# Optimization experiments

Measured on AMD Instinct MI355X. Metric: run time of the kernel, lower is better.

## Reference

```python
import jax, jax.numpy as jnp
import numpy as np

D_MODEL = 1024
N_HEADS = 16
D_HEAD = D_MODEL // N_HEADS
B, T = 2, 2048


def setup_inputs() -> dict:
    key = jax.random.key(0)
    k1, k2, k3 = jax.random.split(key, 3)
    x = jax.random.normal(k1, (B, T, D_MODEL), dtype=jnp.float32)
    # torch nn.Linear weights: y = x @ W.T, W has shape [out, in]
    W_qkv = jax.random.normal(k2, (3 * D_MODEL, D_MODEL), dtype=jnp.float32) * (1.0 / np.sqrt(D_MODEL))
    W_out = jax.random.normal(k3, (D_MODEL, D_MODEL), dtype=jnp.float32) * (1.0 / np.sqrt(D_MODEL))
    return {"x": x, "W_qkv": W_qkv, "W_out": W_out}


def reference(x, W_qkv, W_out):
    Bb, Tt, Dd = x.shape
    qkv = (x @ W_qkv.T).reshape(Bb, Tt, 3, N_HEADS, D_HEAD)
    q, k, v = qkv[:, :, 0], qkv[:, :, 1], qkv[:, :, 2]  # [B,T,H,d]
    q = q.transpose(0, 2, 1, 3)  # [B,H,T,d]
    k = k.transpose(0, 2, 1, 3)
    v = v.transpose(0, 2, 1, 3)
    scale = 1.0 / np.sqrt(D_HEAD)
    scores = jnp.einsum('bhqd,bhkd->bhqk', q, k) * scale  # [B,H,T,T]
    causal = jnp.tril(jnp.ones((Tt, Tt), dtype=bool))
    scores = jnp.where(causal, scores, -jnp.inf)
    A = jax.nn.softmax(scores, axis=-1)
    AV = jnp.einsum('bhqk,bhkd->bhqd', A, v)
    AAV = jnp.einsum('bhqk,bhkd->bhqd', A, AV)  # twicing correction
    out = 2.0 * AV - AAV  # [B,H,T,d]
    out = out.transpose(0, 2, 1, 3).reshape(Bb, Tt, Dd)
    return out @ W_out.T
```

## Files before the change

kernel.cpp:

```cpp
#include <hip/hip_runtime.h>
#include <hip/hip_bf16.h>

#define T_SEQ  2048
#define DMODEL 1024
#define NH     16
#define DH     64
#define NTOK   4096
#define QSCALE 0.18033688011112042f
#define M_FIX  16.0f

typedef unsigned short u16;
typedef short s16x8 __attribute__((ext_vector_type(8)));
typedef unsigned short u16x8 __attribute__((ext_vector_type(8)));
typedef float f32x4 __attribute__((ext_vector_type(4)));

__device__ __forceinline__ u16 f2bf(float f) {
  unsigned u = __float_as_uint(f);
  u += 0x7FFFu + ((u >> 16) & 1u);
  return (u16)(u >> 16);
}
__device__ __forceinline__ unsigned pk2(float a, float b) {
  __hip_bfloat162 h = __float22bfloat162_rn(make_float2(a, b));
  unsigned u;
  __builtin_memcpy(&u, &h, 4);
  return u;
}
__device__ __forceinline__ unsigned pk2z(float a, float b) {
  return __builtin_amdgcn_perm(__float_as_uint(b), __float_as_uint(a), 0x07060302);
}
__device__ __forceinline__ float bf2f(u16 x) {
  return __uint_as_float(((unsigned)x) << 16);
}
__device__ __forceinline__ void async_cp16(const u16* g, u16* l) {
  __builtin_amdgcn_global_load_lds(
      (const __attribute__((address_space(1))) unsigned*)g,
      (__attribute__((address_space(3))) unsigned*)l, 16, 0, 0);
}

__global__ void cast_all(const float* __restrict__ x, const float* __restrict__ wqkv,
                         const float* __restrict__ wout, u16* __restrict__ out) {
  int i = blockIdx.x * blockDim.x + threadIdx.x;
  const float* src; int off;
  if (i < 1048576)      { src = x;    off = 0; }
  else if (i < 1835008) { src = wqkv; off = 1048576; }
  else                  { src = wout; off = 1835008; }
  float4 v = reinterpret_cast<const float4*>(src)[i - off];
  ushort4 r;
  r.x = f2bf(v.x); r.y = f2bf(v.y); r.z = f2bf(v.z); r.w = f2bf(v.w);
  reinterpret_cast<ushort4*>(out)[i] = r;
}

__global__ __launch_bounds__(512, 2) void gemm_qkv(
    const u16* __restrict__ A, const u16* __restrict__ Bm,
    u16* __restrict__ outQ, u16* __restrict__ outK, u16* __restrict__ outV) {
  __shared__ __align__(16) u16 SM[65536];
  const int tid = threadIdx.x, wave = tid >> 6, lane = tid & 63;
  const int f15 = lane & 15, quad = lane >> 4;
  const int bm = blockIdx.x * 256, bn = blockIdx.y * 256;
  const int wm = wave >> 2, wn = wave & 3;
  const int K = DMODEL;

  f32x4 acc[8][4] = {};

  const u16* Ag0 = A  + (size_t)(bm + (2 * wave) * 16 + f15) * K + quad * 8;
  const u16* Ag1 = A  + (size_t)(bm + (2 * wave + 1) * 16 + f15) * K + quad * 8;
  const u16* Bg0 = Bm + (size_t)(bn + (2 * wave) * 16 + f15) * K + quad * 8;
  const u16* Bg1 = Bm + (size_t)(bn + (2 * wave + 1) * 16 + f15) * K + quad * 8;
  u16* LA0 = SM + (2 * wave) * 512 + lane * 8;
  u16* LA1 = SM + (2 * wave + 1) * 512 + lane * 8;
  u16* LB0 = SM + 8192 + (2 * wave) * 512 + lane * 8;
  u16* LB1 = SM + 8192 + (2 * wave + 1) * 512 + lane * 8;

  const int S = K >> 5;
#pragma unroll
  for (int s = 0; s < 3; s++) {
    const int k0 = s * 32, o = s * 16384;
    async_cp16(Ag0 + k0, LA0 + o); async_cp16(Ag1 + k0, LA1 + o);
    async_cp16(Bg0 + k0, LB0 + o); async_cp16(Bg1 + k0, LB1 + o);
  }

  for (int s = 0; s < S; s++) {
    if (s < S - 2)       asm volatile("s_waitcnt vmcnt(8)" ::: "memory");
    else if (s == S - 2) asm volatile("s_waitcnt vmcnt(4)" ::: "memory");
    else                 asm volatile("s_waitcnt vmcnt(0)" ::: "memory");
    __builtin_amdgcn_s_barrier();
    __builtin_amdgcn_sched_barrier(0);
    if (s + 3 < S) {
      const int k0 = (s + 3) * 32, o = ((s + 3) & 3) * 16384;
      async_cp16(Ag0 + k0, LA0 + o); async_cp16(Ag1 + k0, LA1 + o);
      async_cp16(Bg0 + k0, LB0 + o); async_cp16(Bg1 + k0, LB1 + o);
    }
    const u16* Sl = SM + (s & 3) * 16384;
    s16x8 af[8], bfr[4];
#pragma unroll
    for (int ni = 0; ni < 4; ni++)
      bfr[ni] = *reinterpret_cast<const s16x8*>(Sl + 8192 + (wn * 4 + ni) * 512 + lane * 8);
#pragma unroll
    for (int mi = 0; mi < 8; mi++)
      af[mi] = *reinterpret_cast<const s16x8*>(Sl + (wm * 8 + mi) * 512 + lane * 8);
    __builtin_amdgcn_s_setprio(1);
#pragma unroll
    for (int mi = 0; mi < 8; mi++)
#pragma unroll
      for (int ni = 0; ni < 4; ni++)
        acc[mi][ni] = __builtin_amdgcn_mfma_f32_16x16x32_bf16(af[mi], bfr[ni], acc[mi][ni], 0, 0, 0);
    __builtin_amdgcn_s_setprio(0);
  }

  __syncthreads();
  u16* Cs = SM;
  const int ST = 264;
  if (bn < 2048) {
    const float scale = (bn < 1024) ? QSCALE : 1.0f;
#pragma unroll
    for (int c = 0; c < 4; c++) {
      if (c) __syncthreads();
      if (wm == (c >> 1)) {
#pragma unroll
        for (int mi2 = 0; mi2 < 4; mi2++) {
          const int mi = (c & 1) * 4 + mi2;
#pragma unroll
          for (int ni = 0; ni < 4; ni++) {
            const int col = (wn * 4 + ni) * 16 + f15;
#pragma unroll
            for (int r = 0; r < 4; r++)
              Cs[(mi2 * 16 + quad * 4 + r) * ST + col] = f2bf(acc[mi][ni][r] * scale);
          }
        }
      }
      __syncthreads();
      const int row = tid >> 3, cb = (tid & 7) * 32;
      const int gm = bm + c * 64 + row;
#pragma unroll
      for (int c8 = 0; c8 < 4; c8++) {
        const int gc = bn + cb + c8 * 8;
        u16x8 v = *reinterpret_cast<const u16x8*>(&Cs[row * ST + cb + c8 * 8]);
        const int which = gc >> 10, hh = (gc >> 6) & 15, d = gc & 63;
        u16* dst = (which ? outK : outQ) + ((size_t)hh * NTOK + gm) * 64 + d;
        *reinterpret_cast<u16x8*>(dst) = v;
      }
    }
  } else {
    const int bnV = bn - 2048;
#pragma unroll
    for (int c = 0; c < 4; c++) {
      if (c) __syncthreads();
      if (wm == (c >> 1)) {
#pragma unroll
        for (int mi2 = 0; mi2 < 4; mi2++) {
          const int mi = (c & 1) * 4 + mi2;
#pragma unroll
          for (int ni = 0; ni < 4; ni++) {
            const int col = (wn * 4 + ni) * 16 + f15;
#pragma unroll
            for (int r = 0; r < 4; r++)
              Cs[(mi2 * 16 + quad * 4 + r) * ST + col] = f2bf(acc[mi][ni][r]);
          }
        }
      }
      __syncthreads();
      const int fc = tid >> 3, s8 = (tid & 7) * 8;
      const int tb = ((s8 >> 5) & 1) * 32 + ((s8 >> 3) & 3) * 4;
      const int gmb = bm + c * 64;
#pragma unroll
      for (int p = 0; p < 4; p++) {
        const int d = p * 64 + fc;
        u16x8 vv;
#pragma unroll
        for (int j = 0; j < 4; j++) vv[j] = Cs[(tb + j) * ST + d];
#pragma unroll
        for (int j = 0; j < 4; j++) vv[4 + j] = Cs[(tb + 16 + j) * ST + d];
        *reinterpret_cast<u16x8*>(outV + (size_t)(bnV + d) * NTOK + gmb + s8) = vv;
      }
    }
  }
}

__global__ __launch_bounds__(256) void gemm_out(
    const u16* __restrict__ A, const u16* __restrict__ Bm, float* __restrict__ outF) {
  __shared__ __align__(16) u16 SM[18432];
  const int tid = threadIdx.x, wave = tid >> 6, lane = tid & 63;
  const int f15 = lane & 15, quad = lane >> 4;
  const int bm = blockIdx.x * 64, bn = blockIdx.y * 128;
  const int wr = wave >> 1, wc = wave & 1;
  const int K = DMODEL, N = DMODEL;

  f32x4 acc[2][4] = {};

  const u16* Ag = A  + (size_t)(bm + wave * 16 + f15) * K + quad * 8;
  const u16* Bg0 = Bm + (size_t)(bn + (2 * wave) * 16 + f15) * K + quad * 8;
  const u16* Bg1 = Bm + (size_t)(bn + (2 * wave + 1) * 16 + f15) * K + quad * 8;
  u16* LA  = SM + wave * 512 + lane * 8;
  u16* LB0 = SM + 2048 + (2 * wave) * 512 + lane * 8;
  u16* LB1 = SM + 2048 + (2 * wave + 1) * 512 + lane * 8;

  const int KT = K >> 5;
  async_cp16(Ag, LA); async_cp16(Bg0, LB0); async_cp16(Bg1, LB1);
  async_cp16(Ag + 32, LA + 6144); async_cp16(Bg0 + 32, LB0 + 6144); async_cp16(Bg1 + 32, LB1 + 6144);

  int bufr = 0, bufw = 2;
  for (int kt = 0; kt < KT; kt++) {
    if (kt + 1 < KT) asm volatile("s_waitcnt vmcnt(3)" ::: "memory");
    else             asm volatile("s_waitcnt vmcnt(0)" ::: "memory");
    __builtin_amdgcn_s_barrier();
    __builtin_amdgcn_sched_barrier(0);
    if (kt + 2 < KT) {
      const int k0 = (kt + 2) * 32;
      const int o = bufw * 6144;
      async_cp16(Ag + k0, LA + o); async_cp16(Bg0 + k0, LB0 + o); async_cp16(Bg1 + k0, LB1 + o);
    }
    const u16* Af = SM + bufr * 6144;
    const u16* Bf = Af + 2048;
    s16x8 af[2], bfr[4];
#pragma unroll
    for (int mi = 0; mi < 2; mi++)
      af[mi] = *reinterpret_cast<const s16x8*>(Af + (wr * 2 + mi) * 512 + lane * 8);
#pragma unroll
    for (int ni = 0; ni < 4; ni++)
      bfr[ni] = *reinterpret_cast<const s16x8*>(Bf + (wc * 4 + ni) * 512 + lane * 8);
#pragma unroll
    for (int mi = 0; mi < 2; mi++)
#pragma unroll
      for (int ni = 0; ni < 4; ni++)
        acc[mi][ni] = __builtin_amdgcn_mfma_f32_16x16x32_bf16(af[mi], bfr[ni], acc[mi][ni], 0, 0, 0);
    bufr = (bufr == 2) ? 0 : bufr + 1;
    bufw = (bufw == 2) ? 0 : bufw + 1;
  }

#pragma unroll
  for (int mi = 0; mi < 2; mi++)
#pragma unroll
    for (int ni = 0; ni < 4; ni++)
#pragma unroll
      for (int r = 0; r < 4; r++)
        outF[(size_t)(bm + wr * 32 + mi * 16 + quad * 4 + r) * N + bn + wc * 64 + ni * 16 + f15] =
            acc[mi][ni][r];
}

template <int PASS>
__global__ __launch_bounds__(256) void attn_pass(
    const u16* __restrict__ Qb, const u16* __restrict__ Kb, const u16* __restrict__ Vsrc,
    float* __restrict__ LinvG, u16* __restrict__ Vp2, u16* __restrict__ TW) {
  __shared__ __align__(16) u16 SM[16384];
  const int tid = threadIdx.x, wave = tid >> 6, lane = tid & 63;
  const int f15 = lane & 15, quad = lane >> 4;
  const int bid = blockIdx.x;
  const int y = (bid & 7) * 4 + ((bid >> 3) & 3);
  const int b = y >> 4, h = y & 15;
  const int g = bid >> 5;
  const int qt2 = (g < 8) ? (15 - g) : (g - 8);
  const int q0 = qt2 * 128;
  const int ntiles = 2 * qt2 + 2;
  const size_t qk_base = ((size_t)h * NTOK + (size_t)b * T_SEQ) * 64;
  const size_t vt_base = (size_t)h * 64 * NTOK + (size_t)b * T_SEQ;

  s16x8 qf[2][2];
#pragma unroll
  for (int grp = 0; grp < 2; grp++) {
    const u16* qp = Qb + qk_base + (size_t)(q0 + 32 * wave + 16 * grp + f15) * 64 + quad * 8;
    qf[grp][0] = *reinterpret_cast<const s16x8*>(qp);
    qf[grp][1] = *reinterpret_cast<const s16x8*>(qp + 32);
  }
  float invl[2] = {0.f, 0.f};
  if (PASS == 1) {
#pragma unroll
    for (int grp = 0; grp < 2; grp++)
      invl[grp] = LinvG[(size_t)y * T_SEQ + q0 + 32 * wave + 16 * grp + f15];
  }

  f32x4 accO[2][4] = {};
  float l_acc[2] = {0.f, 0.f};

  const u16* Kg = Kb  + qk_base + (size_t)(wave * 16 + f15) * 64 + quad * 8;
  const u16* Vg = Vsrc + vt_base + (size_t)(wave * 16 + f15) * NTOK + quad * 8;
  u16* LK = SM + (wave * 2) * 512 + lane * 8;
  u16* LV = SM + 4096 + (wave * 2) * 512 + lane * 8;

  async_cp16(Kg, LK); async_cp16(Kg + 32, LK + 512);
  async_cp16(Vg, LV); async_cp16(Vg + 32, LV + 512);
  __syncthreads();

  for (int ti = 0; ti < ntiles; ti++) {
    const int buf = ti & 1;
    if (ti + 1 < ntiles) {
      const int j1 = (ti + 1) * 64;
      const int o = (buf ^ 1) * 8192;
      async_cp16(Kg + (size_t)j1 * 64, LK + o);
      async_cp16(Kg + (size_t)j1 * 64 + 32, LK + o + 512);
      async_cp16(Vg + j1, LV + o);
      async_cp16(Vg + j1 + 32, LV + o + 512);
    }
    const u16* Kf = SM + buf * 8192;
    const u16* Vf = SM + buf * 8192 + 4096;
    const int D = (ti - 2 * qt2) * 64;

    if (D < 32 * wave + 32) {
      f32x4 accS[2][4] = {};
#pragma unroll
      for (int st = 0; st < 4; st++) {
        s16x8 k0 = *reinterpret_cast<const s16x8*>(Kf + (st * 2) * 512 + lane * 8);
        s16x8 k1 = *reinterpret_cast<const s16x8*>(Kf + (st * 2 + 1) * 512 + lane * 8);
#pragma unroll
        for (int grp = 0; grp < 2; grp++) {
          accS[grp][st] = __builtin_amdgcn_mfma_f32_16x16x32_bf16(k0, qf[grp][0], accS[grp][st], 0, 0, 0);
          accS[grp][st] = __builtin_amdgcn_mfma_f32_16x16x32_bf16(k1, qf[grp][1], accS[grp][st], 0, 0, 0);
        }
      }
      union pbu { s16x8 v; unsigned u[4]; } pb[2][2];
      if (D + 63 <= 32 * wave) {
#pragma unroll
        for (int grp = 0; grp < 2; grp++)
#pragma unroll
          for (int st = 0; st < 4; st++) {
            float e0 = __builtin_amdgcn_exp2f(accS[grp][st][0] - M_FIX);
            float e1 = __builtin_amdgcn_exp2f(accS[grp][st][1] - M_FIX);
            float e2 = __builtin_amdgcn_exp2f(accS[grp][st][2] - M_FIX);
            float e3 = __builtin_amdgcn_exp2f(accS[grp][st][3] - M_FIX);
            if (PASS == 0) l_acc[grp] += (e0 + e1) + (e2 + e3);
            unsigned w0 = pk2z(e0, e1), w1 = pk2z(e2, e3);
            if (st < 2) { pb[grp][0].u[(st & 1) * 2] = w0; pb[grp][0].u[(st & 1) * 2 + 1] = w1; }
            else        { pb[grp][1].u[(st & 1) * 2] = w0; pb[grp][1].u[(st & 1) * 2 + 1] = w1; }
          }
      } else {
#pragma unroll
        for (int grp = 0; grp < 2; grp++) {
          const int qrel = 32 * wave + 16 * grp + f15;
#pragma unroll
          for (int st = 0; st < 4; st++) {
            const int jb = D + st * 16 + quad * 4;
            float e0 = (jb + 0 <= qrel) ? __builtin_amdgcn_exp2f(accS[grp][st][0] - M_FIX) : 0.f;
            float e1 = (jb + 1 <= qrel) ? __builtin_amdgcn_exp2f(accS[grp][st][1] - M_FIX) : 0.f;
            float e2 = (jb + 2 <= qrel) ? __builtin_amdgcn_exp2f(accS[grp][st][2] - M_FIX) : 0.f;
            float e3 = (jb + 3 <= qrel) ? __builtin_amdgcn_exp2f(accS[grp][st][3] - M_FIX) : 0.f;
            if (PASS == 0) l_acc[grp] += (e0 + e1) + (e2 + e3);
            unsigned w0 = pk2z(e0, e1), w1 = pk2z(e2, e3);
            if (st < 2) { pb[grp][0].u[(st & 1) * 2] = w0; pb[grp][0].u[(st & 1) * 2 + 1] = w1; }
            else        { pb[grp][1].u[(st & 1) * 2] = w0; pb[grp][1].u[(st & 1) * 2 + 1] = w1; }
          }
        }
      }
#pragma unroll
      for (int mt = 0; mt < 4; mt++) {
        s16x8 v0 = *reinterpret_cast<const s16x8*>(Vf + (mt * 2) * 512 + lane * 8);
        s16x8 v1 = *reinterpret_cast<const s16x8*>(Vf + (mt * 2 + 1) * 512 + lane * 8);
#pragma unroll
        for (int grp = 0; grp < 2; grp++) {
          accO[grp][mt] = __builtin_amdgcn_mfma_f32_16x16x32_bf16(v0, pb[grp][0].v, accO[grp][mt], 0, 0, 0);
          accO[grp][mt] = __builtin_amdgcn_mfma_f32_16x16x32_bf16(v1, pb[grp][1].v, accO[grp][mt], 0, 0, 0);
        }
      }
    }
    __syncthreads();
  }

  if (PASS == 0) {
#pragma unroll
    for (int grp = 0; grp < 2; grp++) {
      float l = l_acc[grp];
      l += __shfl_xor(l, 16);
      l += __shfl_xor(l, 32);
      invl[grp] = 1.0f / l;
      if (quad == 0) LinvG[(size_t)y * T_SEQ + q0 + 32 * wave + 16 * grp + f15] = invl[grp];
    }
  }

  if (PASS == 0) {
    u16* E = SM;
#pragma unroll
    for (int g64 = 0; g64 < 2; g64++) {
      __syncthreads();
      if ((wave >> 1) == g64) {
#pragma unroll
        for (int grp = 0; grp < 2; grp++) {
          const int ql = 32 * (wave & 1) + 16 * grp + f15;
          const int slot = (ql >> 5) * 32 + ((ql >> 2) & 3) * 8 + ((ql >> 4) & 1) * 4 + (ql & 3);
#pragma unroll
          for (int mt = 0; mt < 4; mt++)
#pragma unroll
            for (int r = 0; r < 4; r++)
              E[(mt * 16 + quad * 4 + r) * 68 + slot] = f2bf(accO[grp][mt][r] * invl[grp]);
        }
      }
      __syncthreads();
      const int d = tid >> 2, s = (tid & 3) * 16;
      const u16* vg2 = Vsrc + vt_base + (size_t)d * NTOK + q0 + 64 * g64 + s;
      u16* og = Vp2 + vt_base + (size_t)d * NTOK + q0 + 64 * g64 + s;
#pragma unroll
      for (int g2 = 0; g2 < 2; g2++) {
        u16x8 vv = *reinterpret_cast<const u16x8*>(vg2 + g2 * 8);
        u16x8 ee = *reinterpret_cast<const u16x8*>(&E[d * 68 + s + g2 * 8]);
        u16x8 oo;
#pragma unroll
        for (int i = 0; i < 8; i++) oo[i] = f2bf(2.0f * bf2f(vv[i]) - bf2f(ee[i]));
        *reinterpret_cast<u16x8*>(og + g2 * 8) = oo;
      }
    }
  } else {
    u16* E2 = SM;
#pragma unroll
    for (int g64 = 0; g64 < 2; g64++) {
      __syncthreads();
      if ((wave >> 1) == g64) {
#pragma unroll
        for (int grp = 0; grp < 2; grp++) {
          const int ql = 32 * (wave & 1) + 16 * grp + f15;
#pragma unroll
          for (int mt = 0; mt < 4; mt++) {
            uint2 w;
            w.x = pk2(accO[grp][mt][0] * invl[grp], accO[grp][mt][1] * invl[grp]);
            w.y = pk2(accO[grp][mt][2] * invl[grp], accO[grp][mt][3] * invl[grp]);
            *reinterpret_cast<uint2*>(&E2[ql * 72 + mt * 16 + quad * 4]) = w;
          }
        }
      }
      __syncthreads();
      const int q = tid >> 2, s = (tid & 3) * 16;
      u16* dst = TW + ((size_t)b * T_SEQ + q0 + 64 * g64 + q) * DMODEL + h * 64 + s;
      *reinterpret_cast<u16x8*>(dst) = *reinterpret_cast<const u16x8*>(&E2[q * 72 + s]);
      *reinterpret_cast<u16x8*>(dst + 8) = *reinterpret_cast<const u16x8*>(&E2[q * 72 + s + 8]);
    }
  }
}

extern "C" void kernel_launch(void* const* d_in, const int* in_sizes, int n_in,
                              void* d_out, int out_size, void* d_ws, size_t ws_size,
                              hipStream_t stream) {
  const float* x    = (const float*)d_in[0];
  const float* Wqkv = (const float*)d_in[1];
  const float* Wout = (const float*)d_in[2];
  float* out = (float*)d_out;
  char* ws = (char*)d_ws;

  u16*   Xb    = (u16*)(ws + 0);
  u16*   Wqkvb = (u16*)(ws + 8388608);
  u16*   Woutb = (u16*)(ws + 14680064);
  u16*   Qb    = (u16*)(ws + 16777216);
  u16*   Kb    = (u16*)(ws + 25165824);
  u16*   Vtp   = (u16*)(ws + 33554432);
  u16*   TW    = (u16*)(ws + 41943040);
  u16*   Vp2   = (u16*)(ws + 50331648);
  float* LinvG = (float*)(ws + 58720256);

  cast_all<<<8192, 256, 0, stream>>>(x, Wqkv, Wout, Xb);

  gemm_qkv<<<dim3(16, 12), 512, 0, stream>>>(Xb, Wqkvb, Qb, Kb, Vtp);

  attn_pass<0><<<512, 256, 0, stream>>>(Qb, Kb, Vtp, LinvG, Vp2, nullptr);
  attn_pass<1><<<512, 256, 0, stream>>>(Qb, Kb, Vp2, LinvG, nullptr, TW);

  gemm_out<<<dim3(64, 8), 256, 0, stream>>>(TW, Woutb, out);
}
```

Measured before the change: 220.6 us.

## Triple-buffer K/V tiles in attention pass with one barrier per iteration

Changes the attention K/V staging from double to triple buffering, prefetching two tiles ahead with partial vmcnt waits. It keeps a single barrier per iteration instead of a __syncthreads after compute, which lets loads overlap compute more deeply. The cost is 48KB of LDS instead of 32KB, which may reduce occupancy, and correctness now depends on the vmcnt counting being exact.

```diff
diff --git a/kernel.cpp b/kernel.cpp
--- a/kernel.cpp
+++ b/kernel.cpp
@@ -241,7 +241,7 @@
 __global__ __launch_bounds__(256) void attn_pass(
     const u16* __restrict__ Qb, const u16* __restrict__ Kb, const u16* __restrict__ Vsrc,
     float* __restrict__ LinvG, u16* __restrict__ Vp2, u16* __restrict__ TW) {
-  __shared__ __align__(16) u16 SM[16384];
+  __shared__ __align__(16) u16 SM[24576];
   const int tid = threadIdx.x, wave = tid >> 6, lane = tid & 63;
   const int f15 = lane & 15, quad = lane >> 4;
   const int bid = blockIdx.x;
@@ -276,22 +276,26 @@
   u16* LK = SM + (wave * 2) * 512 + lane * 8;
   u16* LV = SM + 4096 + (wave * 2) * 512 + lane * 8;
 
-  async_cp16(Kg, LK); async_cp16(Kg + 32, LK + 512);
-  async_cp16(Vg, LV); async_cp16(Vg + 32, LV + 512);
-  __syncthreads();
+#define ATTN_STAGE(t_) do { \
+    const int j_ = (t_) * 64, o_ = ((t_) % 3) * 8192; \
+    async_cp16(Kg + (size_t)j_ * 64, LK + o_); \
+    async_cp16(Kg + (size_t)j_ * 64 + 32, LK + o_ + 512); \
+    async_cp16(Vg + j_, LV + o_); \
+    async_cp16(Vg + j_ + 32, LV + o_ + 512); \
+  } while (0)
+
+  ATTN_STAGE(0);
+  ATTN_STAGE(1);
 
   for (int ti = 0; ti < ntiles; ti++) {
-    const int buf = ti & 1;
-    if (ti + 1 < ntiles) {
-      const int j1 = (ti + 1) * 64;
-      const int o = (buf ^ 1) * 8192;
-      async_cp16(Kg + (size_t)j1 * 64, LK + o);
-      async_cp16(Kg + (size_t)j1 * 64 + 32, LK + o + 512);
-      async_cp16(Vg + j1, LV + o);
-      async_cp16(Vg + j1 + 32, LV + o + 512);
-    }
-    const u16* Kf = SM + buf * 8192;
-    const u16* Vf = SM + buf * 8192 + 4096;
+    if (ti + 1 < ntiles) asm volatile("s_waitcnt vmcnt(4)" ::: "memory");
+    else                 asm volatile("s_waitcnt vmcnt(0)" ::: "memory");
+    __builtin_amdgcn_s_barrier();
+    __builtin_amdgcn_sched_barrier(0);
+    if (ti + 2 < ntiles) ATTN_STAGE(ti + 2);
+
+    const u16* Kf = SM + (ti % 3) * 8192;
+    const u16* Vf = Kf + 4096;
     const int D = (ti - 2 * qt2) * 64;
 
     if (D < 32 * wave + 32) {
@@ -350,8 +354,8 @@
         }
       }
     }
-    __syncthreads();
-  }
+  }
+#undef ATTN_STAGE
 
   if (PASS == 0) {
 #pragma unroll
```

New measurement: 223.6 us. About the same (+1.4%).

## Restructure QKV GEMM main loop into ping-pong double-stage schedule with interleaved barriers

Applied to the files above, without the earlier changes.

Reworks the QKV projection GEMM k-loop to process two k-stages per iteration. A-fragment LDS reads are split into four sub-phases, each followed by a barrier, so waves alternate between LDS reads and MFMA bursts. Async global-to-LDS copies for the next two stages are issued together once per outer iteration. The aim is to overlap LDS traffic and MFMA across waves and cut per-stage waitcnt overhead, at the cost of many more barriers and a more fragile wait-count schedule.

```diff
diff --git a/kernel.cpp b/kernel.cpp
--- a/kernel.cpp
+++ b/kernel.cpp
@@ -71,41 +71,63 @@
   u16* LB0 = SM + 8192 + (2 * wave) * 512 + lane * 8;
   u16* LB1 = SM + 8192 + (2 * wave + 1) * 512 + lane * 8;
 
-  const int S = K >> 5;
-#pragma unroll
-  for (int s = 0; s < 3; s++) {
-    const int k0 = s * 32, o = s * 16384;
-    async_cp16(Ag0 + k0, LA0 + o); async_cp16(Ag1 + k0, LA1 + o);
-    async_cp16(Bg0 + k0, LB0 + o); async_cp16(Bg1 + k0, LB1 + o);
-  }
-
-  for (int s = 0; s < S; s++) {
-    if (s < S - 2)       asm volatile("s_waitcnt vmcnt(8)" ::: "memory");
-    else if (s == S - 2) asm volatile("s_waitcnt vmcnt(4)" ::: "memory");
-    else                 asm volatile("s_waitcnt vmcnt(0)" ::: "memory");
-    __builtin_amdgcn_s_barrier();
-    __builtin_amdgcn_sched_barrier(0);
-    if (s + 3 < S) {
-      const int k0 = (s + 3) * 32, o = ((s + 3) & 3) * 16384;
-      async_cp16(Ag0 + k0, LA0 + o); async_cp16(Ag1 + k0, LA1 + o);
-      async_cp16(Bg0 + k0, LB0 + o); async_cp16(Bg1 + k0, LB1 + o);
-    }
-    const u16* Sl = SM + (s & 3) * 16384;
-    s16x8 af[8], bfr[4];
-#pragma unroll
-    for (int ni = 0; ni < 4; ni++)
-      bfr[ni] = *reinterpret_cast<const s16x8*>(Sl + 8192 + (wn * 4 + ni) * 512 + lane * 8);
-#pragma unroll
-    for (int mi = 0; mi < 8; mi++)
-      af[mi] = *reinterpret_cast<const s16x8*>(Sl + (wm * 8 + mi) * 512 + lane * 8);
-    __builtin_amdgcn_s_setprio(1);
-#pragma unroll
-    for (int mi = 0; mi < 8; mi++)
-#pragma unroll
-      for (int ni = 0; ni < 4; ni++)
-        acc[mi][ni] = __builtin_amdgcn_mfma_f32_16x16x32_bf16(af[mi], bfr[ni], acc[mi][ni], 0, 0, 0);
-    __builtin_amdgcn_s_setprio(0);
-  }
+#define QKV_STAGE(s_) do { \
+    const int k0_ = (s_) * 32, o_ = ((s_) & 3) * 16384; \
+    async_cp16(Ag0 + k0_, LA0 + o_); async_cp16(Ag1 + k0_, LA1 + o_); \
+    async_cp16(Bg0 + k0_, LB0 + o_); async_cp16(Bg1 + k0_, LB1 + o_); \
+  } while (0)
+
+  QKV_STAGE(0); QKV_STAGE(1); QKV_STAGE(2); QKV_STAGE(3);
+  asm volatile("s_waitcnt vmcnt(8)" ::: "memory");
+  __builtin_amdgcn_s_barrier();
+  __builtin_amdgcn_sched_barrier(0);
+
+  for (int T = 0; T < 16; T++) {
+    const u16* S0 = SM + ((2 * T) & 3) * 16384;
+    const u16* S1 = SM + ((2 * T + 1) & 3) * 16384;
+    s16x8 bfr0[4], bfr1[4];
+#pragma unroll
+    for (int ni = 0; ni < 4; ni++) {
+      bfr0[ni] = *reinterpret_cast<const s16x8*>(S0 + 8192 + (wn * 4 + ni) * 512 + lane * 8);
+      bfr1[ni] = *reinterpret_cast<const s16x8*>(S1 + 8192 + (wn * 4 + ni) * 512 + lane * 8);
+    }
+#pragma unroll
+    for (int q = 0; q < 4; q++) {
+      s16x8 a00 = *reinterpret_cast<const s16x8*>(S0 + (wm * 8 + 2 * q) * 512 + lane * 8);
+      s16x8 a10 = *reinterpret_cast<const s16x8*>(S0 + (wm * 8 + 2 * q + 1) * 512 + lane * 8);
+      s16x8 a01 = *reinterpret_cast<const s16x8*>(S1 + (wm * 8 + 2 * q) * 512 + lane * 8);
+      s16x8 a11 = *reinterpret_cast<const s16x8*>(S1 + (wm * 8 + 2 * q + 1) * 512 + lane * 8);
+      asm volatile("s_waitcnt lgkmcnt(0)" ::: "memory");
+      __builtin_amdgcn_s_barrier();
+      if (q == 3) {
+        __builtin_amdgcn_sched_barrier(0);
+        if (T <= 13) { QKV_STAGE(2 * T + 4); QKV_STAGE(2 * T + 5); }
+      }
+      __builtin_amdgcn_s_setprio(1);
+#pragma unroll
+      for (int ni = 0; ni < 4; ni++) {
+        acc[2 * q][ni]     = __builtin_amdgcn_mfma_f32_16x16x32_bf16(a00, bfr0[ni], acc[2 * q][ni], 0, 0, 0);
+        acc[2 * q + 1][ni] = __builtin_amdgcn_mfma_f32_16x16x32_bf16(a10, bfr0[ni], acc[2 * q + 1][ni], 0, 0, 0);
+      }
+#pragma unroll
+      for (int ni = 0; ni < 4; ni++) {
+        acc[2 * q][ni]     = __builtin_amdgcn_mfma_f32_16x16x32_bf16(a01, bfr1[ni], acc[2 * q][ni], 0, 0, 0);
+        acc[2 * q + 1][ni] = __builtin_amdgcn_mfma_f32_16x16x32_bf16(a11, bfr1[ni], acc[2 * q + 1][ni], 0, 0, 0);
+      }
+      __builtin_amdgcn_s_setprio(0);
+      if (q < 3) {
+        __builtin_amdgcn_s_barrier();
+      } else {
+        if (T <= 13)      asm volatile("s_waitcnt vmcnt(8)" ::: "memory");
+        else if (T == 14) asm volatile("s_waitcnt vmcnt(0)" ::: "memory");
+        if (T < 15) {
+          __builtin_amdgcn_s_barrier();
+          __builtin_amdgcn_sched_barrier(0);
+        }
+      }
+    }
+  }
+#undef QKV_STAGE
 
   __syncthreads();
   u16* Cs = SM;
```

Result: slower. 231.5 us (+4.9%).

## Shrink QKV GEMM N-tile to 192 to fill more CUs

Applied to the files above, without the earlier changes.

The QKV projection GEMM's N-tile shrinks from 256 to 192 columns, raising the grid from 192 to 256 blocks so all CUs on the MI355X get work instead of leaving many idle. The load schedule, wait counts and LDS layout are reworked because waves now load unequal amounts of B. The epilogue is merged so a tile can straddle the K/V boundary, with Q scaling applied per column. In exchange each block does less reuse per K-step and the epilogue has more branching.

```diff
diff --git a/kernel.cpp b/kernel.cpp
--- a/kernel.cpp
+++ b/kernel.cpp
@@ -53,48 +53,54 @@
 __global__ __launch_bounds__(512, 2) void gemm_qkv(
     const u16* __restrict__ A, const u16* __restrict__ Bm,
     u16* __restrict__ outQ, u16* __restrict__ outK, u16* __restrict__ outV) {
-  __shared__ __align__(16) u16 SM[65536];
+  __shared__ __align__(16) u16 SM[57344];
   const int tid = threadIdx.x, wave = tid >> 6, lane = tid & 63;
   const int f15 = lane & 15, quad = lane >> 4;
-  const int bm = blockIdx.x * 256, bn = blockIdx.y * 256;
+  const int bm = blockIdx.x * 256, bn = blockIdx.y * 192;
   const int wm = wave >> 2, wn = wave & 3;
   const int K = DMODEL;
 
-  f32x4 acc[8][4] = {};
-
-  const u16* Ag0 = A  + (size_t)(bm + (2 * wave) * 16 + f15) * K + quad * 8;
-  const u16* Ag1 = A  + (size_t)(bm + (2 * wave + 1) * 16 + f15) * K + quad * 8;
-  const u16* Bg0 = Bm + (size_t)(bn + (2 * wave) * 16 + f15) * K + quad * 8;
-  const u16* Bg1 = Bm + (size_t)(bn + (2 * wave + 1) * 16 + f15) * K + quad * 8;
+  f32x4 acc[8][3] = {};
+
+  const u16* Ag0 = A + (size_t)(bm + (2 * wave) * 16 + f15) * K + quad * 8;
+  const u16* Ag1 = A + (size_t)(bm + (2 * wave + 1) * 16 + f15) * K + quad * 8;
+  const int bf0 = (wave < 4) ? (2 * wave) : (wave + 4);
+  const int bf1 = 2 * wave + 1;
+  const u16* Bg0 = Bm + (size_t)(bn + bf0 * 16 + f15) * K + quad * 8;
+  const u16* Bg1 = Bm + (size_t)(bn + bf1 * 16 + f15) * K + quad * 8;
   u16* LA0 = SM + (2 * wave) * 512 + lane * 8;
   u16* LA1 = SM + (2 * wave + 1) * 512 + lane * 8;
-  u16* LB0 = SM + 8192 + (2 * wave) * 512 + lane * 8;
-  u16* LB1 = SM + 8192 + (2 * wave + 1) * 512 + lane * 8;
+  u16* LB0 = SM + 8192 + bf0 * 512 + lane * 8;
+  u16* LB1 = SM + 8192 + bf1 * 512 + lane * 8;
+
+#define QKV_STAGE(s_) do { \
+    const int k0_ = (s_) * 32, o_ = ((s_) & 3) * 14336; \
+    async_cp16(Ag0 + k0_, LA0 + o_); async_cp16(Ag1 + k0_, LA1 + o_); \
+    async_cp16(Bg0 + k0_, LB0 + o_); \
+    if (wave < 4) async_cp16(Bg1 + k0_, LB1 + o_); \
+  } while (0)
 
   const int S = K >> 5;
-#pragma unroll
-  for (int s = 0; s < 3; s++) {
-    const int k0 = s * 32, o = s * 16384;
-    async_cp16(Ag0 + k0, LA0 + o); async_cp16(Ag1 + k0, LA1 + o);
-    async_cp16(Bg0 + k0, LB0 + o); async_cp16(Bg1 + k0, LB1 + o);
-  }
+  QKV_STAGE(0); QKV_STAGE(1); QKV_STAGE(2);
 
   for (int s = 0; s < S; s++) {
-    if (s < S - 2)       asm volatile("s_waitcnt vmcnt(8)" ::: "memory");
-    else if (s == S - 2) asm volatile("s_waitcnt vmcnt(4)" ::: "memory");
-    else                 asm volatile("s_waitcnt vmcnt(0)" ::: "memory");
+    if (s < S - 2) {
+      if (wave < 4) asm volatile("s_waitcnt vmcnt(8)" ::: "memory");
+      else          asm volatile("s_waitcnt vmcnt(6)" ::: "memory");
+    } else if (s == S - 2) {
+      if (wave < 4) asm volatile("s_waitcnt vmcnt(4)" ::: "memory");
+      else          asm volatile("s_waitcnt vmcnt(3)" ::: "memory");
+    } else {
+      asm volatile("s_waitcnt vmcnt(0)" ::: "memory");
+    }
     __builtin_amdgcn_s_barrier();
     __builtin_amdgcn_sched_barrier(0);
-    if (s + 3 < S) {
-      const int k0 = (s + 3) * 32, o = ((s + 3) & 3) * 16384;
-      async_cp16(Ag0 + k0, LA0 + o); async_cp16(Ag1 + k0, LA1 + o);
-      async_cp16(Bg0 + k0, LB0 + o); async_cp16(Bg1 + k0, LB1 + o);
-    }
-    const u16* Sl = SM + (s & 3) * 16384;
-    s16x8 af[8], bfr[4];
-#pragma unroll
-    for (int ni = 0; ni < 4; ni++)
-      bfr[ni] = *reinterpret_cast<const s16x8*>(Sl + 8192 + (wn * 4 + ni) * 512 + lane * 8);
+    if (s + 3 < S) QKV_STAGE(s + 3);
+    const u16* Sl = SM + (s & 3) * 14336;
+    s16x8 af[8], bfr[3];
+#pragma unroll
+    for (int ni = 0; ni < 3; ni++)
+      bfr[ni] = *reinterpret_cast<const s16x8*>(Sl + 8192 + (wn * 3 + ni) * 512 + lane * 8);
 #pragma unroll
     for (int mi = 0; mi < 8; mi++)
       af[mi] = *reinterpret_cast<const s16x8*>(Sl + (wm * 8 + mi) * 512 + lane * 8);
@@ -102,75 +108,65 @@
 #pragma unroll
     for (int mi = 0; mi < 8; mi++)
 #pragma unroll
-      for (int ni = 0; ni < 4; ni++)
+      for (int ni = 0; ni < 3; ni++)
         acc[mi][ni] = __builtin_amdgcn_mfma_f32_16x16x32_bf16(af[mi], bfr[ni], acc[mi][ni], 0, 0, 0);
     __builtin_amdgcn_s_setprio(0);
   }
+#undef QKV_STAGE
 
   __syncthreads();
   u16* Cs = SM;
-  const int ST = 264;
-  if (bn < 2048) {
-    const float scale = (bn < 1024) ? QSCALE : 1.0f;
-#pragma unroll
-    for (int c = 0; c < 4; c++) {
-      if (c) __syncthreads();
-      if (wm == (c >> 1)) {
-#pragma unroll
-        for (int mi2 = 0; mi2 < 4; mi2++) {
-          const int mi = (c & 1) * 4 + mi2;
-#pragma unroll
-          for (int ni = 0; ni < 4; ni++) {
-            const int col = (wn * 4 + ni) * 16 + f15;
-#pragma unroll
-            for (int r = 0; r < 4; r++)
-              Cs[(mi2 * 16 + quad * 4 + r) * ST + col] = f2bf(acc[mi][ni][r] * scale);
-          }
-        }
-      }
-      __syncthreads();
-      const int row = tid >> 3, cb = (tid & 7) * 32;
+  const int ST = 200;
+  const bool hasQK = (bn < 2048);
+  const bool hasV  = (bn + 192 > 2048);
+#pragma unroll
+  for (int c = 0; c < 4; c++) {
+    if (c) __syncthreads();
+    if (wm == (c >> 1)) {
+#pragma unroll
+      for (int mi2 = 0; mi2 < 4; mi2++) {
+        const int mi = (c & 1) * 4 + mi2;
+#pragma unroll
+        for (int ni = 0; ni < 3; ni++) {
+          const int col = (wn * 3 + ni) * 16 + f15;
+          const float sc = (bn + col < 1024) ? QSCALE : 1.0f;
+#pragma unroll
+          for (int r = 0; r < 4; r++)
+            Cs[(mi2 * 16 + quad * 4 + r) * ST + col] = f2bf(acc[mi][ni][r] * sc);
+        }
+      }
+    }
+    __syncthreads();
+    if (hasQK) {
+      const int row = tid >> 3, cs = (tid & 7) * 24;
       const int gm = bm + c * 64 + row;
 #pragma unroll
-      for (int c8 = 0; c8 < 4; c8++) {
-        const int gc = bn + cb + c8 * 8;
-        u16x8 v = *reinterpret_cast<const u16x8*>(&Cs[row * ST + cb + c8 * 8]);
-        const int which = gc >> 10, hh = (gc >> 6) & 15, d = gc & 63;
-        u16* dst = (which ? outK : outQ) + ((size_t)hh * NTOK + gm) * 64 + d;
-        *reinterpret_cast<u16x8*>(dst) = v;
-      }
-    }
-  } else {
-    const int bnV = bn - 2048;
-#pragma unroll
-    for (int c = 0; c < 4; c++) {
-      if (c) __syncthreads();
-      if (wm == (c >> 1)) {
-#pragma unroll
-        for (int mi2 = 0; mi2 < 4; mi2++) {
-          const int mi = (c & 1) * 4 + mi2;
-#pragma unroll
-          for (int ni = 0; ni < 4; ni++) {
-            const int col = (wn * 4 + ni) * 16 + f15;
-#pragma unroll
-            for (int r = 0; r < 4; r++)
-              Cs[(mi2 * 16 + quad * 4 + r) * ST + col] = f2bf(acc[mi][ni][r]);
-          }
-        }
-      }
-      __syncthreads();
+      for (int c8 = 0; c8 < 3; c8++) {
+        const int gc = bn + cs + c8 * 8;
+        if (gc < 2048) {
+          u16x8 v = *reinterpret_cast<const u16x8*>(&Cs[row * ST + cs + c8 * 8]);
+          const int which = gc >> 10, hh = (gc >> 6) & 15, d = gc & 63;
+          u16* dst = (which ? outK : outQ) + ((size_t)hh * NTOK + gm) * 64 + d;
+          *reinterpret_cast<u16x8*>(dst) = v;
+        }
+      }
+    }
+    if (hasV) {
       const int fc = tid >> 3, s8 = (tid & 7) * 8;
       const int tb = ((s8 >> 5) & 1) * 32 + ((s8 >> 3) & 3) * 4;
       const int gmb = bm + c * 64;
 #pragma unroll
-      for (int p = 0; p < 4; p++) {
+      for (int p = 0; p < 3; p++) {
         const int d = p * 64 + fc;
-        u16x8 vv;
-#pragma unroll
-        for (int j = 0; j < 4; j++) vv[j] = Cs[(tb + j) * ST + d];
-#pragma unroll
-        for (int j = 0; j < 4; j++) vv[4 + j] = Cs[(tb + 16 + j) * ST + d];
-        *reinterpret_cast<u16x8*>(outV + (size_t)(bnV + d) * NTOK + gmb + s8) = vv;
+        const int gcd = bn + d;
+        if (gcd >= 2048) {
+          u16x8 vv;
+#pragma unroll
+          for (int j = 0; j < 4; j++) vv[j] = Cs[(tb + j) * ST + d];
+#pragma unroll
+          for (int j = 0; j < 4; j++) vv[4 + j] = Cs[(tb + 16 + j) * ST + d];
+          *reinterpret_cast<u16x8*>(outV + (size_t)(gcd - 2048) * NTOK + gmb + s8) = vv;
+        }
       }
     }
   }
@@ -443,7 +439,7 @@
 
   cast_all<<<8192, 256, 0, stream>>>(x, Wqkv, Wout, Xb);
 
-  gemm_qkv<<<dim3(16, 12), 512, 0, stream>>>(Xb, Wqkvb, Qb, Kb, Vtp);
+  gemm_qkv<<<dim3(16, 16), 512, 0, stream>>>(Xb, Wqkvb, Qb, Kb, Vtp);
 
   attn_pass<0><<<512, 256, 0, stream>>>(Qb, Kb, Vtp, LinvG, Vp2, nullptr);
   attn_pass<1><<<512, 256, 0, stream>>>(Qb, Kb, Vp2, LinvG, nullptr, TW);
```

Result: faster. 216.1 us (-2.0%).
